# Optimization experiments

Measured on AMD Instinct MI355X. Metric: run time of the kernel, lower is better.

The kernel has to match this reference:

```python
import jax, jax.numpy as jnp
import numpy as np

EPS = 1e-12
NEG = -1e30


def setup_inputs() -> dict:
    key = jax.random.key(0)
    ks = jax.random.split(key, 7)
    B, Nq, Lp, H, D = 96, 35, 180, 768, 128
    q_hidden = jax.random.normal(ks[0], (B, Nq, H), dtype=jnp.float32)
    pos_hidden = jax.random.normal(ks[1], (B, Lp, H), dtype=jnp.float32)
    neg_hidden = jax.random.normal(ks[2], (B, Lp, H), dtype=jnp.float32)
    W = jax.random.normal(ks[3], (H, D), dtype=jnp.float32) * 0.02
    b = jax.random.normal(ks[4], (D,), dtype=jnp.float32) * 0.02
    # non-punctuation filter mask; guarantee at least one valid token per passage
    pos_mask = jax.random.bernoulli(ks[5], 0.85, (B, Lp)).at[:, 0].set(True)
    neg_mask = jax.random.bernoulli(ks[6], 0.85, (B, Lp)).at[:, 0].set(True)
    return {"q_hidden": q_hidden, "pos_hidden": pos_hidden, "neg_hidden": neg_hidden,
            "W": W, "b": b, "pos_mask": pos_mask, "neg_mask": neg_mask}


def _vector_representation(h, W, b):
    # Linear projection then F.normalize(x) with torch default dim=1,
    # i.e. normalization over the SEQUENCE axis (faithful to source).
    x = jnp.einsum('blh,hd->bld', h, W) + b
    norm = jnp.maximum(jnp.sqrt(jnp.sum(x * x, axis=1, keepdims=True)), EPS)
    return x / norm


def _late_interaction(q, p, mask):
    # q: [Bq, Nq, D], p: [Bp, Lp, D], mask: [Bp, Lp] (True = keep token)
    sim = jnp.einsum('qnd,pld->qpnl', q, p)          # [Bq, Bp, Nq, Lp]
    sim = jnp.where(mask[None, :, None, :], sim, NEG)
    return jnp.max(sim, axis=-1).sum(axis=-1)        # MaxSim: max over Lp, sum over Nq


def reference(q_hidden, pos_hidden, neg_hidden, W, b, pos_mask, neg_mask):
    q = _vector_representation(q_hidden, W, b)
    pos = _vector_representation(pos_hidden, W, b)
    neg = _vector_representation(neg_hidden, W, b)
    pos_scores = _late_interaction(q, pos, pos_mask)
    neg_scores = _late_interaction(q, neg, neg_mask)
    return jnp.concatenate((pos_scores, neg_scores), axis=1)  # [B, 2B]
```

## Files before the change

### kernel.cpp

```cpp
#include <hip/hip_runtime.h>

typedef __attribute__((ext_vector_type(4))) float f32x4;
typedef __attribute__((ext_vector_type(8))) short s16x8;
typedef __attribute__((ext_vector_type(4))) short s16x4;
typedef __bf16 bf16x4 __attribute__((ext_vector_type(4)));

#define B_   96
#define NQ   35
#define LP   180
#define H_   768
#define D_   128
#define NEGF (-1e30f)

#define NROWS 37920
#define QROWS 3360
#define PROWS 17280

__device__ __forceinline__ unsigned short f2bf(float f) {
    return __builtin_bit_cast(unsigned short, (__bf16)f);
}

__device__ __forceinline__ s16x4 cvt_bf4(f32x4 v) {
    return __builtin_bit_cast(s16x4, __builtin_convertvector(v, bf16x4));
}

__device__ __forceinline__ s16x8 pack_bf16(f32x4 v0, f32x4 v1) {
    bf16x4 h0 = __builtin_convertvector(v0, bf16x4);
    bf16x4 h1 = __builtin_convertvector(v1, bf16x4);
    s16x4 a = __builtin_bit_cast(s16x4, h0), b = __builtin_bit_cast(s16x4, h1);
    return __builtin_shufflevector(a, b, 0, 1, 2, 3, 4, 5, 6, 7);
}

__device__ __forceinline__ void glds16(const void* g, void* l) {
    __builtin_amdgcn_global_load_lds(
        (const __attribute__((address_space(1))) unsigned int*)g,
        (__attribute__((address_space(3))) unsigned int*)l,
        16, 0, 0);
}

__global__ __launch_bounds__(256) void prep_k(
    const float* __restrict__ W, unsigned short* __restrict__ wthi,
    const unsigned int* __restrict__ pmask_w, unsigned int* __restrict__ ctrl,
    float* __restrict__ ssq) {
    __shared__ unsigned int rr[256];
    int b = blockIdx.x, t = threadIdx.x;
    if (b < 48) {
        int tid = b * 256 + t;
        int nt = tid / (24 * 64);
        int r = tid - nt * 24 * 64;
        int ks = r / 64, lane = r - ks * 64;
        int m = lane & 15, quad = lane >> 4;
        unsigned short* o = wthi + (size_t)tid * 8;
#pragma unroll
        for (int j = 0; j < 8; j++) {
            int k = ks * 32 + quad * 8 + j;
            o[j] = f2bf(W[(size_t)k * D_ + nt * 16 + m]);
        }
    } else if (b < 192) {
        ssq[(b - 48) * 256 + t] = 0.f;
    } else {
        unsigned int f1 = 0, f3 = 0, f4 = 0;
        for (int w = t; w < 4320; w += 256) {
            unsigned int v = pmask_w[w];
            f1 |= v & 0x0000ff00u;
            f3 |= v & 0xff000000u;
            if (w & 1) f4 |= v & 0x000000ffu;
        }
        rr[t] = f1; __syncthreads();
        for (int s2 = 128; s2; s2 >>= 1) { if (t < s2) rr[t] |= rr[t + s2]; __syncthreads(); }
        if (!t) ctrl[0] = rr[0];
        __syncthreads();
        rr[t] = f3; __syncthreads();
        for (int s2 = 128; s2; s2 >>= 1) { if (t < s2) rr[t] |= rr[t + s2]; __syncthreads(); }
        if (!t) ctrl[1] = rr[0];
        __syncthreads();
        rr[t] = f4; __syncthreads();
        for (int s2 = 128; s2; s2 >>= 1) { if (t < s2) rr[t] |= rr[t + s2]; __syncthreads(); }
        if (!t) ctrl[2] = rr[0];
    }
}

__global__ __launch_bounds__(256) void proj_k(
    const float* __restrict__ qh, const float* __restrict__ ph, const float* __restrict__ nh,
    const unsigned short* __restrict__ wthi, const float* __restrict__ bias,
    float* __restrict__ x, float* __restrict__ ssq,
    const void* __restrict__ pm, const void* __restrict__ nm,
    const unsigned int* __restrict__ ctrl, unsigned char* __restrict__ maskc) {
    __shared__ unsigned short sh[2560];
    int b = blockIdx.x;
    if (b >= 2370) {
        int i = (b - 2370) * 256 + threadIdx.x;
        const void* src = (i < B_ * LP) ? pm : nm;
        int j = (i < B_ * LP) ? i : i - B_ * LP;
        unsigned int c1 = ctrl[0], c3 = ctrl[1], c4 = ctrl[2];
        bool bit;
        if (c1 > 0)       bit = ((const unsigned char*)src)[j] != 0;
        else if (c3 > 0)  bit = ((const float*)src)[j] != 0.0f;
        else if (c4 > 0)  bit = ((const int*)src)[j] != 0;
        else              bit = ((const long long*)src)[j] != 0;
        maskc[i] = bit ? 1 : 0;
        return;
    }
    int t = threadIdx.x;
    int wave = t >> 6, lane = t & 63;
    const float* src; int row0l; int growbase;
    if (b < 210)       { src = qh; row0l = b * 16;          growbase = row0l; }
    else if (b < 1290) { src = ph; row0l = (b - 210) * 16;  growbase = QROWS + row0l; }
    else               { src = nh; row0l = (b - 1290) * 16; growbase = QROWS + PROWS + row0l; }
    int m = lane & 15, quad = lane >> 4;

    int srow = t >> 4, c = t & 15;
    int sksg = c >> 3, kk = c & 7;
    int woff = sksg * 640 + srow * 40 + kk * 4;
    int roff = m * 40 + quad * 8;
    const float* gp = src + (size_t)(row0l + srow) * H_ + c * 4;

    f32x4 acc[2];
    acc[0] = (f32x4){0.f, 0.f, 0.f, 0.f};
    acc[1] = (f32x4){0.f, 0.f, 0.f, 0.f};

    int nt0 = wave * 2, nt1 = wave * 2 + 1;

    f32x4 pv = *(const f32x4*)gp;

#pragma unroll 2
    for (int s = 0; s < 12; s++) {
        int bufo = (s & 1) * 1280;
        *(s16x4*)&sh[bufo + woff] = cvt_bf4(pv);
        __syncthreads();
        if (s < 11) pv = *(const f32x4*)(gp + (s + 1) * 64);
#pragma unroll
        for (int ksg = 0; ksg < 2; ksg++) {
            int ksgg = s * 2 + ksg;
            s16x8 a0 = *(const s16x8*)&sh[bufo + ksg * 640 + roff];
            s16x8 bh0 = *(const s16x8*)(wthi + ((size_t)(nt0 * 24 + ksgg) * 64 + lane) * 8);
            s16x8 bh1 = *(const s16x8*)(wthi + ((size_t)(nt1 * 24 + ksgg) * 64 + lane) * 8);
            acc[0] = __builtin_amdgcn_mfma_f32_16x16x32_bf16(a0, bh0, acc[0], 0, 0, 0);
            acc[1] = __builtin_amdgcn_mfma_f32_16x16x32_bf16(a0, bh1, acc[1], 0, 0, 0);
        }
    }

    int base = growbase;
    int bk0, bk1, b1start;
    if (base < QROWS)              { bk0 = base / 35;  bk1 = (base + 15) / 35;
                                     b1start = bk1 * 35; }
    else if (base < QROWS + PROWS) { int r0 = base - QROWS;
                                     bk0 = 96 + r0 / 180;  bk1 = 96 + (r0 + 15) / 180;
                                     b1start = QROWS + (bk1 - 96) * 180; }
    else                           { int r0 = base - QROWS - PROWS;
                                     bk0 = 192 + r0 / 180; bk1 = 192 + (r0 + 15) / 180;
                                     b1start = QROWS + PROWS + (bk1 - 192) * 180; }
#pragma unroll
    for (int ntl = 0; ntl < 2; ntl++) {
        int col = (wave * 2 + ntl) * 16 + m;
        float bv = bias[col];
        f32x4 s4 = acc[ntl];
        float slo = 0.f, shi = 0.f;
#pragma unroll
        for (int r = 0; r < 4; r++) {
            int grow = base + quad * 4 + r;
            float v = s4[r] + bv;
            x[(size_t)grow * D_ + col] = v;
            float v2 = v * v;
            if (bk1 > bk0 && grow >= b1start) shi += v2; else slo += v2;
        }
        slo += __shfl_xor(slo, 16); slo += __shfl_xor(slo, 32);
        if (quad == 0) atomicAdd(ssq + (size_t)bk0 * D_ + col, slo);
        if (bk1 > bk0) {
            shi += __shfl_xor(shi, 16); shi += __shfl_xor(shi, 32);
            if (quad == 0) atomicAdd(ssq + (size_t)bk1 * D_ + col, shi);
        }
    }
}

__global__ __launch_bounds__(256) void scatter_k(
    const float* __restrict__ x, const float* __restrict__ ssq,
    const unsigned char* __restrict__ maskc,
    unsigned short* __restrict__ qfrag, unsigned short* __restrict__ pfrag) {
    int c = blockIdx.x * 256 + threadIdx.x;
    int lane = c & 63, ks = (c >> 6) & 3;
    int quad = lane >> 4, mm = lane & 15;
    int d0 = ks * 32 + quad * 8;
    if (c < 61440) {
        int g = c >> 8;
        int mt = g % 5, qp = g / 5;
        int prow = mt * 16 + mm;
        s16x8 outv = (s16x8){0, 0, 0, 0, 0, 0, 0, 0};
        if (prow < 70) {
            int hi = prow >= 35;
            int bq = qp * 2 + hi;
            int l = prow - hi * 35;
            size_t row = (size_t)bq * 35 + l;
            const f32x4* px = (const f32x4*)(x + row * D_ + d0);
            f32x4 v0 = px[0], v1 = px[1];
            const f32x4* pq = (const f32x4*)(ssq + (size_t)bq * D_ + d0);
            f32x4 q0 = pq[0], q1 = pq[1];
            f32x4 r0, r1;
#pragma unroll
            for (int j = 0; j < 4; j++) {
                r0[j] = rsqrtf(fmaxf(q0[j], 1e-24f));
                r1[j] = rsqrtf(fmaxf(q1[j], 1e-24f));
            }
            outv = pack_bf16(v0 * r0, v1 * r1);
        }
        *(s16x8*)(qfrag + (size_t)c * 8) = outv;
    } else {
        int c2 = c - 61440;
        int g = c2 >> 8;
        int nt = g % 12, pbk = g / 12;
        int l = nt * 16 + mm;
        int lsrc = (l < LP && maskc[pbk * LP + l]) ? l : 0;
        size_t row = QROWS + (size_t)pbk * LP + lsrc;
        const f32x4* px = (const f32x4*)(x + row * D_ + d0);
        f32x4 v0 = px[0], v1 = px[1];
        const f32x4* pq = (const f32x4*)(ssq + (size_t)(96 + pbk) * D_ + d0);
        f32x4 q0 = pq[0], q1 = pq[1];
        f32x4 r0, r1;
#pragma unroll
        for (int j = 0; j < 4; j++) {
            r0[j] = rsqrtf(fmaxf(q0[j], 1e-24f));
            r1[j] = rsqrtf(fmaxf(q1[j], 1e-24f));
        }
        *(s16x8*)(pfrag + (size_t)c2 * 8) = pack_bf16(v0 * r0, v1 * r1);
    }
}

__global__ __launch_bounds__(256, 3) void interact_k(
    const unsigned short* __restrict__ qfrag, const unsigned short* __restrict__ pfrag,
    float* __restrict__ out) {
    __shared__ unsigned short plds[24576];
    int wave = threadIdx.x >> 6, lane = threadIdx.x & 63;
    int b = blockIdx.x;
    int xcd = b & 7, i = b >> 3;
    int c = xcd * 24 + (i % 24);
    int qg = i / 24;
    int side = c / 96, pb = c - side * 96;
    int qp = qg * 4 + wave;
    int m = lane & 15, quad = lane >> 4;

    const unsigned short* pbase = pfrag + (size_t)c * 24576;
    const unsigned short* qbase = qfrag + (size_t)qp * 10240;

#pragma unroll
    for (int ntl = 0; ntl < 3; ntl++) {
        int nt = wave * 3 + ntl;
#pragma unroll
        for (int ks = 0; ks < 4; ks++)
            glds16(pbase + ((size_t)(nt * 4 + ks) * 64 + lane) * 8,
                   &plds[(size_t)(nt * 4 + ks) * 512]);
    }

    s16x8 a[5][4];
#pragma unroll
    for (int mt = 0; mt < 5; mt++)
#pragma unroll
        for (int ks = 0; ks < 4; ks++)
            a[mt][ks] = *(const s16x8*)(qbase + ((size_t)(mt * 4 + ks) * 64 + lane) * 8);

    __syncthreads();

    const f32x4 zero4 = (f32x4){0.f, 0.f, 0.f, 0.f};
    float rmax[5][4];
#pragma unroll
    for (int mt = 0; mt < 5; mt++)
#pragma unroll
        for (int rr = 0; rr < 4; rr++) rmax[mt][rr] = NEGF;

    for (int nt = 0; nt < 12; nt++) {
        s16x8 bfr[4];
#pragma unroll
        for (int ks = 0; ks < 4; ks++)
            bfr[ks] = *(const s16x8*)&plds[((size_t)(nt * 4 + ks) * 64 + lane) * 8];
#pragma unroll
        for (int mt = 0; mt < 5; mt++) {
            f32x4 acc = __builtin_amdgcn_mfma_f32_16x16x32_bf16(a[mt][0], bfr[0], zero4, 0, 0, 0);
            acc = __builtin_amdgcn_mfma_f32_16x16x32_bf16(a[mt][1], bfr[1], acc, 0, 0, 0);
            acc = __builtin_amdgcn_mfma_f32_16x16x32_bf16(a[mt][2], bfr[2], acc, 0, 0, 0);
            acc = __builtin_amdgcn_mfma_f32_16x16x32_bf16(a[mt][3], bfr[3], acc, 0, 0, 0);
#pragma unroll
            for (int rr = 0; rr < 4; rr++)
                rmax[mt][rr] = fmaxf(rmax[mt][rr], acc[rr]);
        }
    }

#pragma unroll
    for (int mt = 0; mt < 5; mt++)
#pragma unroll
        for (int rr = 0; rr < 4; rr++) {
            float v = rmax[mt][rr];
            v = fmaxf(v, __shfl_xor(v, 1));
            v = fmaxf(v, __shfl_xor(v, 2));
            v = fmaxf(v, __shfl_xor(v, 4));
            v = fmaxf(v, __shfl_xor(v, 8));
            rmax[mt][rr] = v;
        }
    float s0 = 0.f, s1 = 0.f;
#pragma unroll
    for (int mt = 0; mt < 5; mt++)
#pragma unroll
        for (int rr = 0; rr < 4; rr++) {
            int prow = mt * 16 + quad * 4 + rr;
            float v = rmax[mt][rr];
            if (prow < 35) s0 += v;
            else if (prow < 70) s1 += v;
        }
    s0 += __shfl_xor(s0, 16); s0 += __shfl_xor(s0, 32);
    s1 += __shfl_xor(s1, 16); s1 += __shfl_xor(s1, 32);
    if (lane == 0) {
        int qb0 = qp * 2, qb1 = qp * 2 + 1;
        out[(size_t)qb0 * (2 * B_) + side * B_ + pb] = s0;
        out[(size_t)qb1 * (2 * B_) + side * B_ + pb] = s1;
    }
}

extern "C" void kernel_launch(void* const* d_in, const int* in_sizes, int n_in,
                              void* d_out, int out_size, void* d_ws, size_t ws_size,
                              hipStream_t stream) {
    const float* qh   = (const float*)d_in[0];
    const float* ph   = (const float*)d_in[1];
    const float* nh   = (const float*)d_in[2];
    const float* W    = (const float*)d_in[3];
    const float* bias = (const float*)d_in[4];
    const void* pmask = d_in[5];
    const void* nmask = d_in[6];
    float* out = (float*)d_out;
    char* ws = (char*)d_ws;

    constexpr size_t CTRL_OFF  = 0;
    constexpr size_t WTHI_OFF  = 256;
    constexpr size_t MASKC_OFF = WTHI_OFF + 196608;
    constexpr size_t SSQ_OFF   = 231424;
    constexpr size_t X_OFF     = SSQ_OFF + 147456;
    constexpr size_t QFRAG_OFF = X_OFF + (size_t)NROWS * D_ * 4;
    constexpr size_t PFRAG_OFF = QFRAG_OFF + 983040;

    unsigned int* ctrl     = (unsigned int*)(ws + CTRL_OFF);
    unsigned short* wthi   = (unsigned short*)(ws + WTHI_OFF);
    unsigned char* maskc   = (unsigned char*)(ws + MASKC_OFF);
    float* ssq             = (float*)(ws + SSQ_OFF);
    float* x               = (float*)(ws + X_OFF);
    unsigned short* qfrag  = (unsigned short*)(ws + QFRAG_OFF);
    unsigned short* pfrag  = (unsigned short*)(ws + PFRAG_OFF);

    prep_k<<<193, 256, 0, stream>>>(W, wthi, (const unsigned int*)pmask, ctrl, ssq);
    proj_k<<<2370 + 135, 256, 0, stream>>>(qh, ph, nh, wthi, bias, x, ssq,
                                           pmask, nmask, ctrl, maskc);
    scatter_k<<<2544, 256, 0, stream>>>(x, ssq, maskc, qfrag, pfrag);
    interact_k<<<2304, 256, 0, stream>>>(qfrag, pfrag, out);
}
```

Measured before the change: 213.0 us.

## Fuse projection, sequence normalization and fragment scatter into one per-passage kernel

```diff
diff --git a/kernel.cpp b/kernel.cpp
--- a/kernel.cpp
+++ b/kernel.cpp
@@ -20,10 +20,6 @@
     return __builtin_bit_cast(unsigned short, (__bf16)f);
 }
 
-__device__ __forceinline__ s16x4 cvt_bf4(f32x4 v) {
-    return __builtin_bit_cast(s16x4, __builtin_convertvector(v, bf16x4));
-}
-
 __device__ __forceinline__ s16x8 pack_bf16(f32x4 v0, f32x4 v1) {
     bf16x4 h0 = __builtin_convertvector(v0, bf16x4);
     bf16x4 h1 = __builtin_convertvector(v1, bf16x4);
@@ -40,8 +36,8 @@
 
 __global__ __launch_bounds__(256) void prep_k(
     const float* __restrict__ W, unsigned short* __restrict__ wthi,
-    const unsigned int* __restrict__ pmask_w, unsigned int* __restrict__ ctrl,
-    float* __restrict__ ssq) {
+    const void* __restrict__ pm, const void* __restrict__ nm,
+    unsigned char* __restrict__ maskc) {
     __shared__ unsigned int rr[256];
     int b = blockIdx.x, t = threadIdx.x;
     if (b < 48) {
@@ -56,172 +52,212 @@
             int k = ks * 32 + quad * 8 + j;
             o[j] = f2bf(W[(size_t)k * D_ + nt * 16 + m]);
         }
-    } else if (b < 192) {
-        ssq[(b - 48) * 256 + t] = 0.f;
     } else {
+        const unsigned int* pw = (const unsigned int*)pm;
         unsigned int f1 = 0, f3 = 0, f4 = 0;
         for (int w = t; w < 4320; w += 256) {
-            unsigned int v = pmask_w[w];
+            unsigned int v = pw[w];
             f1 |= v & 0x0000ff00u;
             f3 |= v & 0xff000000u;
             if (w & 1) f4 |= v & 0x000000ffu;
         }
         rr[t] = f1; __syncthreads();
         for (int s2 = 128; s2; s2 >>= 1) { if (t < s2) rr[t] |= rr[t + s2]; __syncthreads(); }
-        if (!t) ctrl[0] = rr[0];
-        __syncthreads();
+        unsigned int c1 = rr[0]; __syncthreads();
         rr[t] = f3; __syncthreads();
         for (int s2 = 128; s2; s2 >>= 1) { if (t < s2) rr[t] |= rr[t + s2]; __syncthreads(); }
-        if (!t) ctrl[1] = rr[0];
-        __syncthreads();
+        unsigned int c3 = rr[0]; __syncthreads();
         rr[t] = f4; __syncthreads();
         for (int s2 = 128; s2; s2 >>= 1) { if (t < s2) rr[t] |= rr[t + s2]; __syncthreads(); }
-        if (!t) ctrl[2] = rr[0];
-    }
-}
-
-__global__ __launch_bounds__(256) void proj_k(
-    const float* __restrict__ qh, const float* __restrict__ ph, const float* __restrict__ nh,
-    const unsigned short* __restrict__ wthi, const float* __restrict__ bias,
-    float* __restrict__ x, float* __restrict__ ssq,
-    const void* __restrict__ pm, const void* __restrict__ nm,
-    const unsigned int* __restrict__ ctrl, unsigned char* __restrict__ maskc) {
-    __shared__ unsigned short sh[2560];
-    int b = blockIdx.x;
-    if (b >= 2370) {
-        int i = (b - 2370) * 256 + threadIdx.x;
+        unsigned int c4 = rr[0];
+        int i = (b - 48) * 256 + t;
         const void* src = (i < B_ * LP) ? pm : nm;
         int j = (i < B_ * LP) ? i : i - B_ * LP;
-        unsigned int c1 = ctrl[0], c3 = ctrl[1], c4 = ctrl[2];
         bool bit;
         if (c1 > 0)       bit = ((const unsigned char*)src)[j] != 0;
         else if (c3 > 0)  bit = ((const float*)src)[j] != 0.0f;
         else if (c4 > 0)  bit = ((const int*)src)[j] != 0;
         else              bit = ((const long long*)src)[j] != 0;
         maskc[i] = bit ? 1 : 0;
-        return;
-    }
-    int t = threadIdx.x;
-    int wave = t >> 6, lane = t & 63;
-    const float* src; int row0l; int growbase;
-    if (b < 210)       { src = qh; row0l = b * 16;          growbase = row0l; }
-    else if (b < 1290) { src = ph; row0l = (b - 210) * 16;  growbase = QROWS + row0l; }
-    else               { src = nh; row0l = (b - 1290) * 16; growbase = QROWS + PROWS + row0l; }
-    int m = lane & 15, quad = lane >> 4;
-
-    int srow = t >> 4, c = t & 15;
-    int sksg = c >> 3, kk = c & 7;
-    int woff = sksg * 640 + srow * 40 + kk * 4;
-    int roff = m * 40 + quad * 8;
-    const float* gp = src + (size_t)(row0l + srow) * H_ + c * 4;
-
-    f32x4 acc[2];
-    acc[0] = (f32x4){0.f, 0.f, 0.f, 0.f};
-    acc[1] = (f32x4){0.f, 0.f, 0.f, 0.f};
-
-    int nt0 = wave * 2, nt1 = wave * 2 + 1;
-
-    f32x4 pv = *(const f32x4*)gp;
-
-#pragma unroll 2
-    for (int s = 0; s < 12; s++) {
-        int bufo = (s & 1) * 1280;
-        *(s16x4*)&sh[bufo + woff] = cvt_bf4(pv);
-        __syncthreads();
-        if (s < 11) pv = *(const f32x4*)(gp + (s + 1) * 64);
-#pragma unroll
-        for (int ksg = 0; ksg < 2; ksg++) {
-            int ksgg = s * 2 + ksg;
-            s16x8 a0 = *(const s16x8*)&sh[bufo + ksg * 640 + roff];
-            s16x8 bh0 = *(const s16x8*)(wthi + ((size_t)(nt0 * 24 + ksgg) * 64 + lane) * 8);
-            s16x8 bh1 = *(const s16x8*)(wthi + ((size_t)(nt1 * 24 + ksgg) * 64 + lane) * 8);
-            acc[0] = __builtin_amdgcn_mfma_f32_16x16x32_bf16(a0, bh0, acc[0], 0, 0, 0);
-            acc[1] = __builtin_amdgcn_mfma_f32_16x16x32_bf16(a0, bh1, acc[1], 0, 0, 0);
-        }
-    }
-
-    int base = growbase;
-    int bk0, bk1, b1start;
-    if (base < QROWS)              { bk0 = base / 35;  bk1 = (base + 15) / 35;
-                                     b1start = bk1 * 35; }
-    else if (base < QROWS + PROWS) { int r0 = base - QROWS;
-                                     bk0 = 96 + r0 / 180;  bk1 = 96 + (r0 + 15) / 180;
-                                     b1start = QROWS + (bk1 - 96) * 180; }
-    else                           { int r0 = base - QROWS - PROWS;
-                                     bk0 = 192 + r0 / 180; bk1 = 192 + (r0 + 15) / 180;
-                                     b1start = QROWS + PROWS + (bk1 - 192) * 180; }
-#pragma unroll
-    for (int ntl = 0; ntl < 2; ntl++) {
-        int col = (wave * 2 + ntl) * 16 + m;
-        float bv = bias[col];
-        f32x4 s4 = acc[ntl];
-        float slo = 0.f, shi = 0.f;
-#pragma unroll
-        for (int r = 0; r < 4; r++) {
-            int grow = base + quad * 4 + r;
-            float v = s4[r] + bv;
-            x[(size_t)grow * D_ + col] = v;
-            float v2 = v * v;
-            if (bk1 > bk0 && grow >= b1start) shi += v2; else slo += v2;
-        }
-        slo += __shfl_xor(slo, 16); slo += __shfl_xor(slo, 32);
-        if (quad == 0) atomicAdd(ssq + (size_t)bk0 * D_ + col, slo);
-        if (bk1 > bk0) {
-            shi += __shfl_xor(shi, 16); shi += __shfl_xor(shi, 32);
-            if (quad == 0) atomicAdd(ssq + (size_t)bk1 * D_ + col, shi);
-        }
-    }
-}
-
-__global__ __launch_bounds__(256) void scatter_k(
-    const float* __restrict__ x, const float* __restrict__ ssq,
+    }
+}
+
+__global__ __launch_bounds__(512, 1) void proj_k(
+    const float* __restrict__ qh, const float* __restrict__ ph, const float* __restrict__ nh,
+    const unsigned short* __restrict__ wthi, const float* __restrict__ bias,
     const unsigned char* __restrict__ maskc,
     unsigned short* __restrict__ qfrag, unsigned short* __restrict__ pfrag) {
-    int c = blockIdx.x * 256 + threadIdx.x;
-    int lane = c & 63, ks = (c >> 6) & 3;
-    int quad = lane >> 4, mm = lane & 15;
-    int d0 = ks * 32 + quad * 8;
-    if (c < 61440) {
-        int g = c >> 8;
-        int mt = g % 5, qp = g / 5;
-        int prow = mt * 16 + mm;
-        s16x8 outv = (s16x8){0, 0, 0, 0, 0, 0, 0, 0};
-        if (prow < 70) {
-            int hi = prow >= 35;
-            int bq = qp * 2 + hi;
-            int l = prow - hi * 35;
-            size_t row = (size_t)bq * 35 + l;
-            const f32x4* px = (const f32x4*)(x + row * D_ + d0);
-            f32x4 v0 = px[0], v1 = px[1];
-            const f32x4* pq = (const f32x4*)(ssq + (size_t)bq * D_ + d0);
-            f32x4 q0 = pq[0], q1 = pq[1];
-            f32x4 r0, r1;
-#pragma unroll
-            for (int j = 0; j < 4; j++) {
-                r0[j] = rsqrtf(fmaxf(q0[j], 1e-24f));
-                r1[j] = rsqrtf(fmaxf(q1[j], 1e-24f));
-            }
-            outv = pack_bf16(v0 * r0, v1 * r1);
-        }
-        *(s16x8*)(qfrag + (size_t)c * 8) = outv;
+    __shared__ float sb[24576];
+    int b = blockIdx.x, t = threadIdx.x;
+    int wave = t >> 6, lane = t & 63;
+    int m = lane & 15, quad = lane >> 4;
+    unsigned short* xb = (unsigned short*)sb;
+
+    if (b < 192) {
+        const float* src = (b < 96) ? ph + (size_t)b * LP * H_
+                                    : nh + (size_t)(b - 96) * LP * H_;
+        const float* gp[6];
+#pragma unroll
+        for (int g = 0; g < 6; g++) {
+            int rl = wave * 24 + g * 4 + (lane >> 4);
+            int rc = rl < LP ? rl : LP - 1;
+            gp[g] = src + (size_t)rc * H_ + (((lane & 15) ^ (2 * (rl & 7))) << 2);
+        }
+
+        f32x4 acc[12];
+#pragma unroll
+        for (int mt = 0; mt < 12; mt++) acc[mt] = (f32x4){0.f, 0.f, 0.f, 0.f};
+
+        {
+            float* d0 = sb + wave * 1536;
+#pragma unroll
+            for (int g = 0; g < 6; g++) glds16(gp[g], d0 + g * 256);
+        }
+        __syncthreads();
+
+        for (int s = 0; s < 12; s++) {
+            if (s < 11) {
+                float* d0 = sb + ((s + 1) & 1) * 12288 + wave * 1536;
+#pragma unroll
+                for (int g = 0; g < 6; g++) glds16(gp[g] + (s + 1) * 64, d0 + g * 256);
+            }
+            const float* bb = sb + (s & 1) * 12288;
+#pragma unroll
+            for (int ksg = 0; ksg < 2; ksg++) {
+                s16x8 bf = *(const s16x8*)(wthi +
+                           ((size_t)(wave * 24 + s * 2 + ksg) * 64 + lane) * 8);
+                int kc = ksg * 8 + quad * 2;
+#pragma unroll
+                for (int mt = 0; mt < 12; mt++) {
+                    int row = mt * 16 + m;
+                    const float* fb = bb + row * 64 + ((kc ^ (2 * (row & 7))) << 2);
+                    f32x4 lo = *(const f32x4*)fb, hi = *(const f32x4*)(fb + 4);
+                    acc[mt] = __builtin_amdgcn_mfma_f32_16x16x32_bf16(
+                        pack_bf16(lo, hi), bf, acc[mt], 0, 0, 0);
+                }
+            }
+            __syncthreads();
+        }
+
+        float bv = bias[wave * 16 + m];
+        float s2 = 0.f;
+#pragma unroll
+        for (int mt = 0; mt < 12; mt++)
+#pragma unroll
+            for (int r = 0; r < 4; r++) {
+                int prow = mt * 16 + quad * 4 + r;
+                float v = acc[mt][r] + bv;
+                acc[mt][r] = v;
+                if (prow < LP) s2 += v * v;
+            }
+        s2 += __shfl_xor(s2, 16); s2 += __shfl_xor(s2, 32);
+        float sc = rsqrtf(fmaxf(s2, 1e-24f));
+        __syncthreads();
+#pragma unroll
+        for (int mt = 0; mt < 12; mt++)
+#pragma unroll
+            for (int r = 0; r < 4; r++) {
+                int prow = mt * 16 + quad * 4 + r;
+                if (prow < LP) xb[prow * 136 + wave * 16 + m] = f2bf(acc[mt][r] * sc);
+            }
+        __syncthreads();
+        const unsigned char* mk = maskc + b * LP;
+        unsigned short* pdst = pfrag + (size_t)b * 24576;
+#pragma unroll
+        for (int i = 0; i < 6; i++) {
+            int ch = t + i * 512;
+            int ln = ch & 63;
+            int l = ((ch >> 8) << 4) + (ln & 15);
+            int lsrc = (l < LP && mk[l]) ? l : 0;
+            int d0 = ((ch >> 6) & 3) * 32 + (ln >> 4) * 8;
+            *(s16x8*)&pdst[(size_t)ch * 8] = *(const s16x8*)&xb[lsrc * 136 + d0];
+        }
     } else {
-        int c2 = c - 61440;
-        int g = c2 >> 8;
-        int nt = g % 12, pbk = g / 12;
-        int l = nt * 16 + mm;
-        int lsrc = (l < LP && maskc[pbk * LP + l]) ? l : 0;
-        size_t row = QROWS + (size_t)pbk * LP + lsrc;
-        const f32x4* px = (const f32x4*)(x + row * D_ + d0);
-        f32x4 v0 = px[0], v1 = px[1];
-        const f32x4* pq = (const f32x4*)(ssq + (size_t)(96 + pbk) * D_ + d0);
-        f32x4 q0 = pq[0], q1 = pq[1];
-        f32x4 r0, r1;
-#pragma unroll
-        for (int j = 0; j < 4; j++) {
-            r0[j] = rsqrtf(fmaxf(q0[j], 1e-24f));
-            r1[j] = rsqrtf(fmaxf(q1[j], 1e-24f));
-        }
-        *(s16x8*)(pfrag + (size_t)c2 * 8) = pack_bf16(v0 * r0, v1 * r1);
+        int qp = b - 192;
+        const float* src = qh + (size_t)qp * 70 * H_;
+        const float* gp[3];
+#pragma unroll
+        for (int g = 0; g < 3; g++) {
+            int rl = wave * 12 + g * 4 + (lane >> 4);
+            int rc = rl < 70 ? rl : 69;
+            gp[g] = src + (size_t)rc * H_ + (((lane & 15) ^ (2 * (rl & 7))) << 2);
+        }
+
+        f32x4 acc[5];
+#pragma unroll
+        for (int mt = 0; mt < 5; mt++) acc[mt] = (f32x4){0.f, 0.f, 0.f, 0.f};
+
+        {
+            float* d0 = sb + wave * 768;
+#pragma unroll
+            for (int g = 0; g < 3; g++) glds16(gp[g], d0 + g * 256);
+        }
+        __syncthreads();
+
+        for (int s = 0; s < 12; s++) {
+            if (s < 11) {
+                float* d0 = sb + ((s + 1) & 1) * 6144 + wave * 768;
+#pragma unroll
+                for (int g = 0; g < 3; g++) glds16(gp[g] + (s + 1) * 64, d0 + g * 256);
+            }
+            const float* bb = sb + (s & 1) * 6144;
+#pragma unroll
+            for (int ksg = 0; ksg < 2; ksg++) {
+                s16x8 bf = *(const s16x8*)(wthi +
+                           ((size_t)(wave * 24 + s * 2 + ksg) * 64 + lane) * 8);
+                int kc = ksg * 8 + quad * 2;
+#pragma unroll
+                for (int mt = 0; mt < 5; mt++) {
+                    int row = mt * 16 + m;
+                    const float* fb = bb + row * 64 + ((kc ^ (2 * (row & 7))) << 2);
+                    f32x4 lo = *(const f32x4*)fb, hi = *(const f32x4*)(fb + 4);
+                    acc[mt] = __builtin_amdgcn_mfma_f32_16x16x32_bf16(
+                        pack_bf16(lo, hi), bf, acc[mt], 0, 0, 0);
+                }
+            }
+            __syncthreads();
+        }
+
+        float bv = bias[wave * 16 + m];
+        float s0 = 0.f, s1 = 0.f;
+#pragma unroll
+        for (int mt = 0; mt < 5; mt++)
+#pragma unroll
+            for (int r = 0; r < 4; r++) {
+                int prow = mt * 16 + quad * 4 + r;
+                float v = acc[mt][r] + bv;
+                acc[mt][r] = v;
+                if (prow < 35) s0 += v * v;
+                else if (prow < 70) s1 += v * v;
+            }
+        s0 += __shfl_xor(s0, 16); s0 += __shfl_xor(s0, 32);
+        s1 += __shfl_xor(s1, 16); s1 += __shfl_xor(s1, 32);
+        float sc0 = rsqrtf(fmaxf(s0, 1e-24f));
+        float sc1 = rsqrtf(fmaxf(s1, 1e-24f));
+        __syncthreads();
+#pragma unroll
+        for (int mt = 0; mt < 5; mt++)
+#pragma unroll
+            for (int r = 0; r < 4; r++) {
+                int prow = mt * 16 + quad * 4 + r;
+                if (prow < 70)
+                    xb[prow * 136 + wave * 16 + m] =
+                        f2bf(acc[mt][r] * (prow < 35 ? sc0 : sc1));
+            }
+        __syncthreads();
+        unsigned short* qdst = qfrag + (size_t)qp * 10240;
+#pragma unroll
+        for (int i = 0; i < 3; i++) {
+            int ch = t + i * 512;
+            if (ch < 1280) {
+                int ln = ch & 63;
+                int prow = ((ch >> 8) << 4) + (ln & 15);
+                int d0 = ((ch >> 6) & 3) * 32 + (ln >> 4) * 8;
+                s16x8 v = (s16x8){0, 0, 0, 0, 0, 0, 0, 0};
+                if (prow < 70) v = *(const s16x8*)&xb[prow * 136 + d0];
+                *(s16x8*)&qdst[(size_t)ch * 8] = v;
+            }
+        }
     }
 }
 
@@ -326,25 +362,17 @@
     float* out = (float*)d_out;
     char* ws = (char*)d_ws;
 
-    constexpr size_t CTRL_OFF  = 0;
     constexpr size_t WTHI_OFF  = 256;
     constexpr size_t MASKC_OFF = WTHI_OFF + 196608;
-    constexpr size_t SSQ_OFF   = 231424;
-    constexpr size_t X_OFF     = SSQ_OFF + 147456;
-    constexpr size_t QFRAG_OFF = X_OFF + (size_t)NROWS * D_ * 4;
+    constexpr size_t QFRAG_OFF = MASKC_OFF + 34560;
     constexpr size_t PFRAG_OFF = QFRAG_OFF + 983040;
 
-    unsigned int* ctrl     = (unsigned int*)(ws + CTRL_OFF);
     unsigned short* wthi   = (unsigned short*)(ws + WTHI_OFF);
     unsigned char* maskc   = (unsigned char*)(ws + MASKC_OFF);
-    float* ssq             = (float*)(ws + SSQ_OFF);
-    float* x               = (float*)(ws + X_OFF);
     unsigned short* qfrag  = (unsigned short*)(ws + QFRAG_OFF);
     unsigned short* pfrag  = (unsigned short*)(ws + PFRAG_OFF);
 
-    prep_k<<<193, 256, 0, stream>>>(W, wthi, (const unsigned int*)pmask, ctrl, ssq);
-    proj_k<<<2370 + 135, 256, 0, stream>>>(qh, ph, nh, wthi, bias, x, ssq,
-                                           pmask, nmask, ctrl, maskc);
-    scatter_k<<<2544, 256, 0, stream>>>(x, ssq, maskc, qfrag, pfrag);
+    prep_k<<<183, 256, 0, stream>>>(W, wthi, pmask, nmask, maskc);
+    proj_k<<<240, 512, 0, stream>>>(qh, ph, nh, wthi, bias, maskc, qfrag, pfrag);
     interact_k<<<2304, 256, 0, stream>>>(qfrag, pfrag, out);
 }
```

Result: faster. 196.2 us (-7.9%).
